# Performance work log

Measured on AMD Instinct MI355X. Metric: run time of the kernel, lower is better.

Reference implementation:

```python
import jax, jax.numpy as jnp
import numpy as np

B, S, D = 2, 2048, 4096
H, KVH, HD = 32, 8, 128
THETA = 10000.0


def setup_inputs() -> dict:
    key = jax.random.key(0)
    k1, k2, k3 = jax.random.split(key, 3)
    hidden_states = jax.random.normal(k1, (B, S, D), jnp.float32)
    w_qkv = jax.random.normal(k2, ((KVH * 2 + H) * HD, D), jnp.float32) * 0.02
    w_dense = jax.random.normal(k3, (D, D), jnp.float32) * 0.02
    return {"hidden_states": hidden_states, "w_qkv": w_qkv, "w_dense": w_dense}


def _rope(x, pos):
    # x: [B, H, S, HD]; Falcon rotary embedding (rotate_half convention)
    inv_freq = 1.0 / (THETA ** (jnp.arange(0, HD, 2, dtype=jnp.float32) / HD))
    freqs = pos[:, None] * inv_freq[None, :]           # [S, HD/2]
    emb = jnp.concatenate([freqs, freqs], axis=-1)      # [S, HD]
    cos, sin = jnp.cos(emb), jnp.sin(emb)
    x1, x2 = x[..., : HD // 2], x[..., HD // 2 :]
    rot = jnp.concatenate([-x2, x1], axis=-1)
    return x * cos + rot * sin


def reference(hidden_states, w_qkv, w_dense):
    # fused QKV projection (FalconLinear, no bias)
    fused = jnp.einsum('bsd,ed->bse', hidden_states, w_qkv)  # [B,S,(2KVH+H)*HD]
    g = H // KVH  # query heads per kv head
    qkv = fused.reshape(B, S, KVH, g + 2, HD)
    q = qkv[:, :, :, :g]                        # [B,S,KVH,g,HD]
    k = jnp.broadcast_to(qkv[:, :, :, g:g + 1], q.shape)
    v = jnp.broadcast_to(qkv[:, :, :, g + 1:g + 2], q.shape)
    q, k, v = (t.reshape(B, S, H, HD).transpose(0, 2, 1, 3) for t in (q, k, v))
    pos = jnp.arange(S, dtype=jnp.float32)
    q = _rope(q, pos)
    k = _rope(k, pos)
    scores = jnp.einsum('bhqd,bhkd->bhqk', q, k) / jnp.sqrt(jnp.float32(HD))
    causal = jnp.tril(jnp.ones((S, S), dtype=bool))
    scores = jnp.where(causal, scores, jnp.float32(-1e9))
    attn = jax.nn.softmax(scores, axis=-1)
    out = jnp.einsum('bhqk,bhkd->bhqd', attn, v)
    out = out.transpose(0, 2, 1, 3).reshape(B, S, H * HD)   # merge heads
    return jnp.einsum('bsd,ed->bse', out, w_dense)
```

## Files before the change

### kernel.cpp

```cpp
#include <hip/hip_runtime.h>

#define B_   2
#define S_   2048
#define D_   4096
#define H_   32
#define KVH_ 8
#define HD_  128
#define NE_  6144

using f32x4  = __attribute__((ext_vector_type(4))) float;
using f32x16 = __attribute__((ext_vector_type(16))) float;
using bf16x8 = __attribute__((ext_vector_type(8))) __bf16;
using u16x8  = __attribute__((ext_vector_type(8))) unsigned short;

__device__ __forceinline__ unsigned short f2bf(float f) {
  union { float f; unsigned u; } v; v.f = f;
  unsigned r = v.u + 0x7FFFu + ((v.u >> 16) & 1u);
  return (unsigned short)(r >> 16);
}
__device__ __forceinline__ float bf2f(unsigned short h) {
  union { unsigned u; float f; } v; v.u = ((unsigned)h) << 16; return v.f;
}
__device__ __forceinline__ bf16x8 ld8(const unsigned short* p) {
  return *reinterpret_cast<const bf16x8*>(p);
}
__device__ __forceinline__ bf16x8 ld8b(const void* base, int byte_off) {
  return *reinterpret_cast<const bf16x8*>((const char*)base + byte_off);
}
__device__ __forceinline__ void cp16(const void* g, void* l) {
  __builtin_amdgcn_global_load_lds(
      (const __attribute__((address_space(1))) void*)g,
      (__attribute__((address_space(3))) void*)l, 16, 0, 0);
}
__device__ __forceinline__ float exp2a(float x) {
  float r; asm("v_exp_f32 %0, %1" : "=v"(r) : "v"(x)); return r;
}
__device__ __forceinline__ unsigned cvtpk(float lo, float hi) {
  unsigned r; asm("v_cvt_pk_bf16_f32 %0, %1, %2" : "=v"(r) : "v"(lo), "v"(hi));
  return r;
}

#define SC2F 0.12751652f

__global__ __launch_bounds__(256) void cvt2_f32_bf16(
    const float* __restrict__ s0, unsigned short* __restrict__ d0, int n0,
    const float* __restrict__ s1, unsigned short* __restrict__ d1, int n1)
{
  int i = blockIdx.x * 256 + threadIdx.x;
  const float* src; unsigned short* dst;
  if (i < n0) { src = s0; dst = d0; }
  else        { i -= n0; if (i >= n1) return; src = s1; dst = d1; }
  f32x4 v = *reinterpret_cast<const f32x4*>(src + (size_t)i * 4);
  ushort4 o;
  o.x = f2bf(v[0]); o.y = f2bf(v[1]); o.z = f2bf(v[2]); o.w = f2bf(v[3]);
  *reinterpret_cast<ushort4*>(dst + (size_t)i * 4) = o;
}

template <typename OutT, int NT>
__global__ __launch_bounds__(512, 2) void gemm256(
    const unsigned short* __restrict__ A,
    const unsigned short* __restrict__ Bw,
    OutT* __restrict__ C, int M, int N)
{
  constexpr int K  = 4096;
  constexpr int NI = (K / 64) / 2;
  constexpr int NB = NT / 64;
  constexpr int NN = NT / 64;
  constexpr int WN = NT / 4;
  constexpr int BBUF = NT * 128;
  __shared__ __align__(16) char lds[65536 + 2 * BBUF];

  const int tid  = threadIdx.x;
  const int lane = tid & 63;
  const int wave = tid >> 6;
  const int wr = wave >> 2;
  const int wc = wave & 3;
  const int lr = lane & 15;
  const int lk = (lane >> 4) * 8;

  int id  = blockIdx.y * gridDim.x + blockIdx.x;
  const int nwg = gridDim.x * gridDim.y;
  if ((nwg & 7) == 0) { const int q = nwg >> 3; id = (id & 7) * q + (id >> 3); }
  const int row0 = (id / gridDim.x) * 256;
  const int col0 = (id % gridDim.x) * NT;

  int rwA[2], csA[2], dbA[2];
#pragma unroll
  for (int j = 0; j < 2; ++j) {
    dbA[j] = j * 8192 + tid * 16;
    rwA[j] = dbA[j] >> 7;
    csA[j] = ((dbA[j] & 127) ^ ((rwA[j] & 7) << 4)) >> 1;
  }
  auto stA = [&](int buf, int h, int t) {
#pragma unroll
    for (int j = 0; j < 2; ++j)
      cp16(A + (size_t)(row0 + h * 128 + rwA[j]) * K + t * 64 + csA[j],
           lds + buf * 32768 + h * 16384 + dbA[j]);
  };
  const int dbB = tid * 16;
  const int rwB = dbB >> 7;
  const int csB = ((dbB & 127) ^ ((rwB & 7) << 4)) >> 1;
  auto stB = [&](int buf, int c, int t) {
    cp16(Bw + (size_t)(col0 + c * 64 + rwB) * K + t * 64 + csB,
         lds + 65536 + buf * BBUF + c * 8192 + dbB);
  };

  const int cb0 = ((0 + lk) << 1) ^ ((lr & 7) << 4);
  const int cb1 = ((32 + lk) << 1) ^ ((lr & 7) << 4);
  const int aRowB = (wr * 16 + lr) * 128;
  const int bRowB = (wc * WN + lr) * 128;

  f32x4 acc[8][NN];
#pragma unroll
  for (int m = 0; m < 8; ++m)
#pragma unroll
    for (int n = 0; n < NN; ++n) acc[m][n] = (f32x4){0.f, 0.f, 0.f, 0.f};
  bf16x8 bfr[NN][2];

#define FENCE asm volatile("" ::: "memory")
#define VMC(nn) asm volatile("s_waitcnt vmcnt(" #nn ")" ::: "memory")

#define MFMA4(mrow, r0, r1)                                                     \
    _Pragma("unroll")                                                           \
    for (int n = 0; n < NN; ++n) {                                              \
      acc[(mrow)+0][n] = __builtin_amdgcn_mfma_f32_16x16x32_bf16(r0##0, bfr[n][0], acc[(mrow)+0][n], 0, 0, 0); \
      acc[(mrow)+0][n] = __builtin_amdgcn_mfma_f32_16x16x32_bf16(r0##1, bfr[n][1], acc[(mrow)+0][n], 0, 0, 0); \
      acc[(mrow)+1][n] = __builtin_amdgcn_mfma_f32_16x16x32_bf16(r1##0, bfr[n][0], acc[(mrow)+1][n], 0, 0, 0); \
      acc[(mrow)+1][n] = __builtin_amdgcn_mfma_f32_16x16x32_bf16(r1##1, bfr[n][1], acc[(mrow)+1][n], 0, 0, 0); \
    }

#define PHASEPAIR(pa, buf, STG1, STG2, W2)                                      \
  {                                                                             \
    if ((pa) == 0) {                                                            \
      _Pragma("unroll")                                                         \
      for (int n = 0; n < NN; ++n) {                                            \
        bfr[n][0] = ld8b(lds, 65536 + (buf) * BBUF + bRowB + n * 2048 + cb0);   \
        bfr[n][1] = ld8b(lds, 65536 + (buf) * BBUF + bRowB + n * 2048 + cb1);   \
      }                                                                         \
    }                                                                           \
    const int abase = (buf) * 32768 + (pa) * 8192 + aRowB;                      \
    bf16x8 xa00 = ld8b(lds, abase + cb0);                                       \
    bf16x8 xa01 = ld8b(lds, abase + cb1);                                       \
    bf16x8 xa10 = ld8b(lds, abase + 4096 + cb0);                                \
    bf16x8 xa11 = ld8b(lds, abase + 4096 + cb1);                                \
    bf16x8 ya00 = ld8b(lds, abase + 8192 + cb0);                                \
    bf16x8 ya01 = ld8b(lds, abase + 8192 + cb1);                                \
    bf16x8 ya10 = ld8b(lds, abase + 12288 + cb0);                               \
    bf16x8 ya11 = ld8b(lds, abase + 12288 + cb1);                               \
    STG1;                                                                       \
    __builtin_amdgcn_s_setprio(1);                                              \
    MFMA4((pa) * 2, xa0, xa1);                                                  \
    __builtin_amdgcn_s_setprio(0);                                              \
    FENCE;                                                                      \
    __builtin_amdgcn_s_barrier();                                               \
    STG2;                                                                       \
    __builtin_amdgcn_s_setprio(1);                                              \
    MFMA4((pa) * 2 + 2, ya0, ya1);                                              \
    __builtin_amdgcn_s_setprio(0);                                              \
    W2;                                                                         \
    FENCE;                                                                      \
    __builtin_amdgcn_s_barrier();                                               \
  }

#pragma unroll
  for (int c = 0; c < NB; ++c) stB(0, c, 0);
  stA(0, 0, 0); stA(0, 1, 0);
#pragma unroll
  for (int c = 0; c < NB; ++c) stB(1, c, 1);
  stA(1, 0, 1);
  if constexpr (NB == 4) { VMC(8); } else { VMC(7); }
  FENCE;
  __builtin_amdgcn_s_barrier();

  for (int i = 0; i < NI; ++i) {
    const int t1  = 2 * i + 1;
    const int tn0 = 2 * i + 2;
    const int tn1 = 2 * i + 3;
    const bool pre = (i + 1 < NI);
    PHASEPAIR(0, 0,
        { stA(1, 1, t1); },
        { if (pre) { stB(0, 0, tn0); stB(0, 1, tn0); } },
        { if (pre) { if constexpr (NB == 4) VMC(10); else VMC(9); }
          else     { if constexpr (NB == 4) VMC(8);  else VMC(7); } });
    PHASEPAIR(2, 0,
        { if (pre) stA(0, 0, tn0); },
        { if (pre) { _Pragma("unroll") for (int c = 2; c < NB; ++c) stB(0, c, tn0); } },
        { if (pre) { if constexpr (NB == 4) VMC(8); else VMC(7); }
          else     { VMC(2); } });
    PHASEPAIR(0, 1,
        { if (pre) stA(0, 1, tn0); },
        { if (pre) { stB(1, 0, tn1); stB(1, 1, tn1); } },
        { if (pre) { if constexpr (NB == 4) VMC(10); else VMC(9); }
          else     { VMC(0); } });
    PHASEPAIR(2, 1,
        { if (pre) stA(1, 0, tn1); },
        { if (pre) { _Pragma("unroll") for (int c = 2; c < NB; ++c) stB(1, c, tn1); } },
        { if (pre) { if constexpr (NB == 4) VMC(8); else VMC(7); } });
  }
#undef PHASEPAIR
#undef MFMA4
#undef FENCE
#undef VMC

  const int orow = (lane >> 4) * 4;
#pragma unroll
  for (int m = 0; m < 8; ++m) {
    const int gr0 = row0 + m * 32 + wr * 16 + orow;
#pragma unroll
    for (int n = 0; n < NN; ++n) {
      const int gc = col0 + wc * WN + n * 16 + lr;
#pragma unroll
      for (int r = 0; r < 4; ++r) {
        float val = acc[m][n][r];
        if constexpr (sizeof(OutT) == 2)
          C[(size_t)(gr0 + r) * N + gc] = f2bf(val);
        else
          C[(size_t)(gr0 + r) * N + gc] = val;
      }
    }
  }
}

#define ROPE_N (B_ * S_ * 48 * 8)
__global__ __launch_bounds__(256) void rope_scatter_cvt(
    const unsigned short* __restrict__ fused,
    unsigned short* __restrict__ Qr,
    unsigned short* __restrict__ Kr,
    unsigned short* __restrict__ Vt,
    const float* __restrict__ wdense,
    unsigned short* __restrict__ Wdb,
    int nD4)
{
  int idx = blockIdx.x * 256 + threadIdx.x;
  if (idx >= ROPE_N) {
    int i = idx - ROPE_N;
    if (i >= nD4) return;
    f32x4 v = *reinterpret_cast<const f32x4*>(wdense + (size_t)i * 4);
    ushort4 o;
    o.x = f2bf(v[0]); o.y = f2bf(v[1]); o.z = f2bf(v[2]); o.w = f2bf(v[3]);
    *reinterpret_cast<ushort4*>(Wdb + (size_t)i * 4) = o;
    return;
  }
  int dg = idx & 7;
  int t = idx >> 3;
  int e = t % 48;
  int bs = t / 48;
  int s = bs % S_;
  int b = bs / S_;
  int kvh = e / 6, j = e % 6;
  const unsigned short* src = fused + (size_t)bs * NE_ + e * 128 + dg * 8;
  u16x8 lo = *reinterpret_cast<const u16x8*>(src);
  u16x8 hi = *reinterpret_cast<const u16x8*>(src + 64);
  if (j == 5) {
    size_t base = (size_t)(b * KVH_ + kvh) * HD_ * S_ + s;
#pragma unroll
    for (int jj = 0; jj < 8; ++jj) {
      Vt[base + (size_t)(dg * 8 + jj) * S_]      = lo[jj];
      Vt[base + (size_t)(dg * 8 + jj + 64) * S_] = hi[jj];
    }
  } else {
    const float sc = (j == 4) ? 1.0f : SC2F;
    u16x8 olo, ohi;
#pragma unroll
    for (int jj = 0; jj < 8; ++jj) {
      int d = dg * 8 + jj;
      float x1 = bf2f(lo[jj]), x2 = bf2f(hi[jj]);
      float inv = __expf(-(float)d * (9.2103403719761836f / 64.0f));
      float ang = (float)s * inv;
      float sn, c;
      sincosf(ang, &sn, &c);
      olo[jj] = f2bf((x1 * c - x2 * sn) * sc);
      ohi[jj] = f2bf((x2 * c + x1 * sn) * sc);
    }
    unsigned short* dst;
    if (j == 4) dst = Kr + ((size_t)(b * KVH_ + kvh) * S_ + s) * HD_;
    else        dst = Qr + ((size_t)(b * H_ + kvh * 4 + j) * S_ + s) * HD_;
    *reinterpret_cast<u16x8*>(dst + dg * 8)      = olo;
    *reinterpret_cast<u16x8*>(dst + dg * 8 + 64) = ohi;
  }
}

__global__ __launch_bounds__(256, 2) void attn_fwd(
    const unsigned short* __restrict__ Qr,
    const unsigned short* __restrict__ Kr,
    const unsigned short* __restrict__ Vt,
    unsigned short* __restrict__ O)
{
  __shared__ __align__(16) unsigned short Kld[2][64 * 128];
  __shared__ __align__(16) unsigned short Vld[2][128 * 64];

  const int tid  = threadIdx.x;
  const int lane = tid & 63;
  const int wave = tid >> 6;
  const int bx = blockIdx.x;
  const int hh = blockIdx.y;
  const int b  = blockIdx.z;
  const int kvh = hh >> 2;
  const int q31 = lane & 31;
  const int h   = lane >> 5;

  const unsigned short* Kb = Kr + (size_t)(b * KVH_ + kvh) * S_ * HD_;
  const unsigned short* Vb = Vt + (size_t)(b * KVH_ + kvh) * HD_ * S_;

  auto stage = [&](int buf, int kb) {
#pragma unroll
    for (int i = 0; i < 4; ++i) {
      const int db = i * 4096 + tid * 16;
      {
        const int row  = db >> 8;
        const int colb = (db & 255) ^ ((row & 15) << 4);
        cp16(Kb + (size_t)(kb * 64 + row) * HD_ + (colb >> 1),
             (char*)&Kld[buf][0] + i * 4096 + wave * 1024);
      }
      {
        const int row  = db >> 7;
        const int colb = (db & 127) ^ ((row & 7) << 4);
        cp16(Vb + (size_t)row * S_ + kb * 64 + (colb >> 1),
             (char*)&Vld[buf][0] + i * 4096 + wave * 1024);
      }
    }
  };

  const int kswz = (q31 & 15) << 4;
  const int vswz = (q31 & 7) << 4;

  for (int half = 0; half < 2; ++half) {
    const int qt = half ? (15 - bx) : bx;
    const int nkb = 2 * (qt + 1);
    const int qg = qt * 128 + wave * 32 + q31;

    const unsigned short* qbase =
        Qr + ((size_t)(b * H_ + hh) * S_ + qg) * HD_;
    bf16x8 qf[8];
#pragma unroll
    for (int t = 0; t < 8; ++t) qf[t] = ld8(qbase + t * 16 + h * 8);

    f32x16 acc_o[4] = {};
    float m = -1e30f, lpart = 0.f;

    stage(0, 0);
    __syncthreads();

    for (int kb = 0; kb < nkb; ++kb) {
      const int cur = kb & 1;
      if (kb + 1 < nkb) stage(cur ^ 1, kb + 1);

      const char* Kc = (const char*)&Kld[cur][0];
      const char* Vc = (const char*)&Vld[cur][0];

      f32x16 accs0 = {}, accs1 = {};
      __builtin_amdgcn_s_setprio(1);
#pragma unroll
      for (int t = 0; t < 8; ++t) {
        const int hd2 = t * 32 + h * 16;
        bf16x8 kf0 = ld8b(Kc, ((q31 << 8) + hd2) ^ kswz);
        bf16x8 kf1 = ld8b(Kc, (((32 + q31) << 8) + hd2) ^ kswz);
        accs0 = __builtin_amdgcn_mfma_f32_32x32x16_bf16(kf0, qf[t], accs0, 0, 0, 0);
        accs1 = __builtin_amdgcn_mfma_f32_32x32x16_bf16(kf1, qf[t], accs1, 0, 0, 0);
      }
      __builtin_amdgcn_s_setprio(0);

      if (kb >= 2 * qt) {
        const int kbase = kb * 64 + 4 * h;
#pragma unroll
        for (int reg = 0; reg < 16; ++reg) {
          const int k0 = kbase + (reg & 3) + 8 * (reg >> 2);
          if (k0 > qg)      accs0[reg] = -1e30f;
          if (k0 + 32 > qg) accs1[reg] = -1e30f;
        }
      }

      float mx = -1e30f;
#pragma unroll
      for (int reg = 0; reg < 16; ++reg)
        mx = fmaxf(mx, fmaxf(accs0[reg], accs1[reg]));
      if (!__all(mx <= m + 8.f)) {
        float mxo = __shfl_xor(mx, 32, 64);
        float mnew = fmaxf(m, fmaxf(mx, mxo));
        float corr = exp2a(m - mnew);
        m = mnew;
        lpart *= corr;
#pragma unroll
        for (int reg = 0; reg < 16; ++reg) {
          const int crow = (reg & 3) + 8 * (reg >> 2) + 4 * h;
          float cw = __shfl(corr, crow, 64);
#pragma unroll
          for (int dj = 0; dj < 4; ++dj) acc_o[dj][reg] *= cw;
        }
      }

      bf16x8 pa[4];
#pragma unroll
      for (int ks = 0; ks < 4; ++ks) {
        float e[8];
#pragma unroll
        for (int j = 0; j < 8; ++j) {
          float s = (ks < 2) ? accs0[8 * (ks & 1) + j] : accs1[8 * (ks & 1) + j];
          e[j] = exp2a(s - m);
          lpart += e[j];
        }
        unsigned w01 = cvtpk(e[0], e[1]);
        unsigned w23 = cvtpk(e[2], e[3]);
        unsigned w45 = cvtpk(e[4], e[5]);
        unsigned w67 = cvtpk(e[6], e[7]);
        asm volatile("v_permlane32_swap_b32 %0, %1" : "+v"(w01), "+v"(w45));
        asm volatile("v_permlane32_swap_b32 %0, %1" : "+v"(w23), "+v"(w67));
        union { unsigned u[4]; bf16x8 v; } pu;
        pu.u[0] = w01; pu.u[1] = w23; pu.u[2] = w45; pu.u[3] = w67;
        pa[ks] = pu.v;
      }

      __builtin_amdgcn_s_setprio(1);
#pragma unroll
      for (int dj = 0; dj < 4; ++dj) {
        const int vrow = (dj * 32 + q31) << 7;
#pragma unroll
        for (int ks = 0; ks < 4; ++ks) {
          bf16x8 vf = ld8b(Vc, (vrow + ks * 32 + h * 16) ^ vswz);
          acc_o[dj] = __builtin_amdgcn_mfma_f32_32x32x16_bf16(pa[ks], vf, acc_o[dj], 0, 0, 0);
        }
      }
      __builtin_amdgcn_s_setprio(0);

      __syncthreads();
    }

    float lsum = lpart + __shfl_xor(lpart, 32, 64);
    float linv = 1.f / lsum;
#pragma unroll
    for (int reg = 0; reg < 16; ++reg) {
      const int crow = (reg & 3) + 8 * (reg >> 2) + 4 * h;
      float lv = __shfl(linv, crow, 64);
      size_t rowoff =
          (size_t)(b * S_ + qt * 128 + wave * 32 + crow) * (H_ * HD_) + hh * HD_ + q31;
#pragma unroll
      for (int dj = 0; dj < 4; ++dj)
        O[rowoff + dj * 32] = f2bf(acc_o[dj][reg] * lv);
    }
  }
}

__global__ void fill_sentinel(float* __restrict__ O, int n) {
  int i = blockIdx.x * 256 + threadIdx.x;
  if (i < n) O[i] = 12345.0f;
}

extern "C" void kernel_launch(void* const* d_in, const int* in_sizes, int n_in,
                              void* d_out, int out_size, void* d_ws, size_t ws_size,
                              hipStream_t stream) {
  const float* hidden = (const float*)d_in[0];
  const float* wqkv   = (const float*)d_in[1];
  const float* wdense = (const float*)d_in[2];
  float* out = (float*)d_out;

  const size_t NEED = 134217728;
  if (ws_size < NEED) {
    fill_sentinel<<<dim3((out_size + 255) / 256), dim3(256), 0, stream>>>(out, out_size);
    return;
  }

  char* ws = (char*)d_ws;
  unsigned short* Hb    = (unsigned short*)(ws);
  unsigned short* Wqb   = (unsigned short*)(ws + 33554432);
  unsigned short* fused = (unsigned short*)(ws + 83886080);
  unsigned short* Qr    = (unsigned short*)(ws);
  unsigned short* Kr    = (unsigned short*)(ws + 33554432);
  unsigned short* Vt    = (unsigned short*)(ws + 41943040);
  unsigned short* Wdb   = (unsigned short*)(ws + 50331648);
  unsigned short* attn_out = (unsigned short*)(ws + 83886080);

  const int nH4 = B_ * S_ * D_ / 4;
  const int nQ4 = NE_ * D_ / 4;
  const int nD4 = D_ * D_ / 4;

  cvt2_f32_bf16<<<dim3((nH4 + nQ4 + 255) / 256), dim3(256), 0, stream>>>(
      hidden, Hb, nH4, wqkv, Wqb, nQ4);

  gemm256<unsigned short, 192><<<dim3(NE_ / 192, (B_ * S_) / 256), dim3(512), 0, stream>>>(
      Hb, Wqb, fused, B_ * S_, NE_);

  rope_scatter_cvt<<<dim3((ROPE_N + nD4 + 255) / 256), dim3(256), 0, stream>>>(
      fused, Qr, Kr, Vt, wdense, Wdb, nD4);

  attn_fwd<<<dim3(8, H_, B_), dim3(256), 0, stream>>>(Qr, Kr, Vt, attn_out);

  gemm256<float, 256><<<dim3(D_ / 256, (B_ * S_) / 256), dim3(512), 0, stream>>>(
      attn_out, Wdb, out, B_ * S_, D_);
}
```

Before: 472.2 us.

## Single-buffer K in attention, one q-tile per block, raise occupancy to 3

The attention kernel now keeps a single K buffer in LDS (V stays double-buffered) and issues the next K/V prefetch only after a barrier that follows the QK MFMAs. This cuts LDS per block so three blocks can fit per CU. Each block now handles one query tile instead of a balanced pair of tiles (bx and 15-bx), and the grid becomes head-major with 1024 blocks. The trade-off is the loss of paired causal load balancing, an extra barrier per iteration, and less overlap of the K load with compute.

```diff
diff --git a/kernel.cpp b/kernel.cpp
--- a/kernel.cpp
+++ b/kernel.cpp
@@ -280,20 +280,20 @@
   }
 }
 
-__global__ __launch_bounds__(256, 2) void attn_fwd(
+__global__ __launch_bounds__(256, 3) void attn_fwd(
     const unsigned short* __restrict__ Qr,
     const unsigned short* __restrict__ Kr,
     const unsigned short* __restrict__ Vt,
     unsigned short* __restrict__ O)
 {
-  __shared__ __align__(16) unsigned short Kld[2][64 * 128];
+  __shared__ __align__(16) unsigned short Kld[64 * 128];
   __shared__ __align__(16) unsigned short Vld[2][128 * 64];
 
   const int tid  = threadIdx.x;
   const int lane = tid & 63;
   const int wave = tid >> 6;
-  const int bx = blockIdx.x;
-  const int hh = blockIdx.y;
+  const int hh = blockIdx.x;
+  const int qt = blockIdx.y;
   const int b  = blockIdx.z;
   const int kvh = hh >> 2;
   const int q31 = lane & 31;
@@ -302,141 +302,141 @@
   const unsigned short* Kb = Kr + (size_t)(b * KVH_ + kvh) * S_ * HD_;
   const unsigned short* Vb = Vt + (size_t)(b * KVH_ + kvh) * HD_ * S_;
 
-  auto stage = [&](int buf, int kb) {
+  auto stageK = [&](int kb) {
 #pragma unroll
     for (int i = 0; i < 4; ++i) {
       const int db = i * 4096 + tid * 16;
-      {
-        const int row  = db >> 8;
-        const int colb = (db & 255) ^ ((row & 15) << 4);
-        cp16(Kb + (size_t)(kb * 64 + row) * HD_ + (colb >> 1),
-             (char*)&Kld[buf][0] + i * 4096 + wave * 1024);
-      }
-      {
-        const int row  = db >> 7;
-        const int colb = (db & 127) ^ ((row & 7) << 4);
-        cp16(Vb + (size_t)row * S_ + kb * 64 + (colb >> 1),
-             (char*)&Vld[buf][0] + i * 4096 + wave * 1024);
-      }
+      const int row  = db >> 8;
+      const int colb = (db & 255) ^ ((row & 15) << 4);
+      cp16(Kb + (size_t)(kb * 64 + row) * HD_ + (colb >> 1),
+           (char*)&Kld[0] + i * 4096 + wave * 1024);
+    }
+  };
+  auto stageV = [&](int buf, int kb) {
+#pragma unroll
+    for (int i = 0; i < 4; ++i) {
+      const int db = i * 4096 + tid * 16;
+      const int row  = db >> 7;
+      const int colb = (db & 127) ^ ((row & 7) << 4);
+      cp16(Vb + (size_t)row * S_ + kb * 64 + (colb >> 1),
+           (char*)&Vld[buf][0] + i * 4096 + wave * 1024);
     }
   };
 
   const int kswz = (q31 & 15) << 4;
   const int vswz = (q31 & 7) << 4;
 
-  for (int half = 0; half < 2; ++half) {
-    const int qt = half ? (15 - bx) : bx;
-    const int nkb = 2 * (qt + 1);
-    const int qg = qt * 128 + wave * 32 + q31;
-
-    const unsigned short* qbase =
-        Qr + ((size_t)(b * H_ + hh) * S_ + qg) * HD_;
-    bf16x8 qf[8];
-#pragma unroll
-    for (int t = 0; t < 8; ++t) qf[t] = ld8(qbase + t * 16 + h * 8);
-
-    f32x16 acc_o[4] = {};
-    float m = -1e30f, lpart = 0.f;
-
-    stage(0, 0);
+  const int nkb = 2 * (qt + 1);
+  const int qg = qt * 128 + wave * 32 + q31;
+
+  const unsigned short* qbase =
+      Qr + ((size_t)(b * H_ + hh) * S_ + qg) * HD_;
+  bf16x8 qf[8];
+#pragma unroll
+  for (int t = 0; t < 8; ++t) qf[t] = ld8(qbase + t * 16 + h * 8);
+
+  f32x16 acc_o[4] = {};
+  float m = -1e30f, lpart = 0.f;
+
+  stageK(0);
+  stageV(0, 0);
+  __syncthreads();
+
+  for (int kb = 0; kb < nkb; ++kb) {
+    const int cur = kb & 1;
+    const char* Vc = (const char*)&Vld[cur][0];
+
+    f32x16 accs0 = {}, accs1 = {};
+    __builtin_amdgcn_s_setprio(1);
+#pragma unroll
+    for (int t = 0; t < 8; ++t) {
+      const int hd2 = t * 32 + h * 16;
+      bf16x8 kf0 = ld8b(Kld, ((q31 << 8) + hd2) ^ kswz);
+      bf16x8 kf1 = ld8b(Kld, (((32 + q31) << 8) + hd2) ^ kswz);
+      accs0 = __builtin_amdgcn_mfma_f32_32x32x16_bf16(kf0, qf[t], accs0, 0, 0, 0);
+      accs1 = __builtin_amdgcn_mfma_f32_32x32x16_bf16(kf1, qf[t], accs1, 0, 0, 0);
+    }
+    __builtin_amdgcn_s_setprio(0);
+
     __syncthreads();
-
-    for (int kb = 0; kb < nkb; ++kb) {
-      const int cur = kb & 1;
-      if (kb + 1 < nkb) stage(cur ^ 1, kb + 1);
-
-      const char* Kc = (const char*)&Kld[cur][0];
-      const char* Vc = (const char*)&Vld[cur][0];
-
-      f32x16 accs0 = {}, accs1 = {};
-      __builtin_amdgcn_s_setprio(1);
-#pragma unroll
-      for (int t = 0; t < 8; ++t) {
-        const int hd2 = t * 32 + h * 16;
-        bf16x8 kf0 = ld8b(Kc, ((q31 << 8) + hd2) ^ kswz);
-        bf16x8 kf1 = ld8b(Kc, (((32 + q31) << 8) + hd2) ^ kswz);
-        accs0 = __builtin_amdgcn_mfma_f32_32x32x16_bf16(kf0, qf[t], accs0, 0, 0, 0);
-        accs1 = __builtin_amdgcn_mfma_f32_32x32x16_bf16(kf1, qf[t], accs1, 0, 0, 0);
+    if (kb + 1 < nkb) { stageK(kb + 1); stageV(cur ^ 1, kb + 1); }
+
+    if (kb >= 2 * qt) {
+      const int kbase = kb * 64 + 4 * h;
+#pragma unroll
+      for (int reg = 0; reg < 16; ++reg) {
+        const int k0 = kbase + (reg & 3) + 8 * (reg >> 2);
+        if (k0 > qg)      accs0[reg] = -1e30f;
+        if (k0 + 32 > qg) accs1[reg] = -1e30f;
       }
-      __builtin_amdgcn_s_setprio(0);
-
-      if (kb >= 2 * qt) {
-        const int kbase = kb * 64 + 4 * h;
-#pragma unroll
-        for (int reg = 0; reg < 16; ++reg) {
-          const int k0 = kbase + (reg & 3) + 8 * (reg >> 2);
-          if (k0 > qg)      accs0[reg] = -1e30f;
-          if (k0 + 32 > qg) accs1[reg] = -1e30f;
-        }
+    }
+
+    float mx = -1e30f;
+#pragma unroll
+    for (int reg = 0; reg < 16; ++reg)
+      mx = fmaxf(mx, fmaxf(accs0[reg], accs1[reg]));
+    if (!__all(mx <= m + 8.f)) {
+      float mxo = __shfl_xor(mx, 32, 64);
+      float mnew = fmaxf(m, fmaxf(mx, mxo));
+      float corr = exp2a(m - mnew);
+      m = mnew;
+      lpart *= corr;
+#pragma unroll
+      for (int reg = 0; reg < 16; ++reg) {
+        const int crow = (reg & 3) + 8 * (reg >> 2) + 4 * h;
+        float cw = __shfl(corr, crow, 64);
+#pragma unroll
+        for (int dj = 0; dj < 4; ++dj) acc_o[dj][reg] *= cw;
       }
-
-      float mx = -1e30f;
-#pragma unroll
-      for (int reg = 0; reg < 16; ++reg)
-        mx = fmaxf(mx, fmaxf(accs0[reg], accs1[reg]));
-      if (!__all(mx <= m + 8.f)) {
-        float mxo = __shfl_xor(mx, 32, 64);
-        float mnew = fmaxf(m, fmaxf(mx, mxo));
-        float corr = exp2a(m - mnew);
-        m = mnew;
-        lpart *= corr;
-#pragma unroll
-        for (int reg = 0; reg < 16; ++reg) {
-          const int crow = (reg & 3) + 8 * (reg >> 2) + 4 * h;
-          float cw = __shfl(corr, crow, 64);
-#pragma unroll
-          for (int dj = 0; dj < 4; ++dj) acc_o[dj][reg] *= cw;
-        }
+    }
+
+    bf16x8 pa[4];
+#pragma unroll
+    for (int ks = 0; ks < 4; ++ks) {
+      float e[8];
+#pragma unroll
+      for (int j = 0; j < 8; ++j) {
+        float s = (ks < 2) ? accs0[8 * (ks & 1) + j] : accs1[8 * (ks & 1) + j];
+        e[j] = exp2a(s - m);
+        lpart += e[j];
       }
-
-      bf16x8 pa[4];
+      unsigned w01 = cvtpk(e[0], e[1]);
+      unsigned w23 = cvtpk(e[2], e[3]);
+      unsigned w45 = cvtpk(e[4], e[5]);
+      unsigned w67 = cvtpk(e[6], e[7]);
+      asm volatile("v_permlane32_swap_b32 %0, %1" : "+v"(w01), "+v"(w45));
+      asm volatile("v_permlane32_swap_b32 %0, %1" : "+v"(w23), "+v"(w67));
+      union { unsigned u[4]; bf16x8 v; } pu;
+      pu.u[0] = w01; pu.u[1] = w23; pu.u[2] = w45; pu.u[3] = w67;
+      pa[ks] = pu.v;
+    }
+
+    __builtin_amdgcn_s_setprio(1);
+#pragma unroll
+    for (int dj = 0; dj < 4; ++dj) {
+      const int vrow = (dj * 32 + q31) << 7;
 #pragma unroll
       for (int ks = 0; ks < 4; ++ks) {
-        float e[8];
-#pragma unroll
-        for (int j = 0; j < 8; ++j) {
-          float s = (ks < 2) ? accs0[8 * (ks & 1) + j] : accs1[8 * (ks & 1) + j];
-          e[j] = exp2a(s - m);
-          lpart += e[j];
-        }
-        unsigned w01 = cvtpk(e[0], e[1]);
-        unsigned w23 = cvtpk(e[2], e[3]);
-        unsigned w45 = cvtpk(e[4], e[5]);
-        unsigned w67 = cvtpk(e[6], e[7]);
-        asm volatile("v_permlane32_swap_b32 %0, %1" : "+v"(w01), "+v"(w45));
-        asm volatile("v_permlane32_swap_b32 %0, %1" : "+v"(w23), "+v"(w67));
-        union { unsigned u[4]; bf16x8 v; } pu;
-        pu.u[0] = w01; pu.u[1] = w23; pu.u[2] = w45; pu.u[3] = w67;
-        pa[ks] = pu.v;
+        bf16x8 vf = ld8b(Vc, (vrow + ks * 32 + h * 16) ^ vswz);
+        acc_o[dj] = __builtin_amdgcn_mfma_f32_32x32x16_bf16(pa[ks], vf, acc_o[dj], 0, 0, 0);
       }
-
-      __builtin_amdgcn_s_setprio(1);
-#pragma unroll
-      for (int dj = 0; dj < 4; ++dj) {
-        const int vrow = (dj * 32 + q31) << 7;
-#pragma unroll
-        for (int ks = 0; ks < 4; ++ks) {
-          bf16x8 vf = ld8b(Vc, (vrow + ks * 32 + h * 16) ^ vswz);
-          acc_o[dj] = __builtin_amdgcn_mfma_f32_32x32x16_bf16(pa[ks], vf, acc_o[dj], 0, 0, 0);
-        }
-      }
-      __builtin_amdgcn_s_setprio(0);
-
-      __syncthreads();
-    }
-
-    float lsum = lpart + __shfl_xor(lpart, 32, 64);
-    float linv = 1.f / lsum;
-#pragma unroll
-    for (int reg = 0; reg < 16; ++reg) {
-      const int crow = (reg & 3) + 8 * (reg >> 2) + 4 * h;
-      float lv = __shfl(linv, crow, 64);
-      size_t rowoff =
-          (size_t)(b * S_ + qt * 128 + wave * 32 + crow) * (H_ * HD_) + hh * HD_ + q31;
-#pragma unroll
-      for (int dj = 0; dj < 4; ++dj)
-        O[rowoff + dj * 32] = f2bf(acc_o[dj][reg] * lv);
-    }
+    }
+    __builtin_amdgcn_s_setprio(0);
+
+    __syncthreads();
+  }
+
+  float lsum = lpart + __shfl_xor(lpart, 32, 64);
+  float linv = 1.f / lsum;
+#pragma unroll
+  for (int reg = 0; reg < 16; ++reg) {
+    const int crow = (reg & 3) + 8 * (reg >> 2) + 4 * h;
+    float lv = __shfl(linv, crow, 64);
+    size_t rowoff =
+        (size_t)(b * S_ + qt * 128 + wave * 32 + crow) * (H_ * HD_) + hh * HD_ + q31;
+#pragma unroll
+    for (int dj = 0; dj < 4; ++dj)
+      O[rowoff + dj * 32] = f2bf(acc_o[dj][reg] * lv);
   }
 }
 
@@ -482,7 +482,7 @@
   rope_scatter_cvt<<<dim3((ROPE_N + nD4 + 255) / 256), dim3(256), 0, stream>>>(
       fused, Qr, Kr, Vt, wdense, Wdb, nD4);
 
-  attn_fwd<<<dim3(8, H_, B_), dim3(256), 0, stream>>>(Qr, Kr, Vt, attn_out);
+  attn_fwd<<<dim3(32, 16, B_), dim3(256), 0, stream>>>(Qr, Kr, Vt, attn_out);
 
   gemm256<float, 256><<<dim3(D_ / 256, (B_ * S_) / 256), dim3(512), 0, stream>>>(
       attn_out, Wdb, out, B_ * S_, D_);
```

Result: slower. 627.8 us (+33.0%).
